# Optimization experiments

Hardware: AMD Instinct MI355X
Metric: run time of the kernel (lower is better)

Reference implementation:

```python
import jax, jax.numpy as jnp
import numpy as np

EMB = 1024
HEADS = 16
HEAD_DIM = EMB // HEADS
B, T = 2, 2048
LN_EPS = 1e-5  # torch nn.LayerNorm default


def _layernorm(x, g, b):
    # LayerNorm over last dim (head_dim), elementwise affine
    mu = jnp.mean(x, axis=-1, keepdims=True)
    var = jnp.mean(jnp.square(x - mu), axis=-1, keepdims=True)
    return (x - mu) * jax.lax.rsqrt(var + LN_EPS) * g + b


def setup_inputs() -> dict:
    key = jax.random.key(0)
    ks = jax.random.split(key, 6)
    sc = 1.0 / np.sqrt(EMB)  # keep linear outputs O(1)
    return {
        "x": jax.random.normal(ks[0], (B, T, EMB), dtype=jnp.float32),
        "Wk": jax.random.normal(ks[1], (EMB, EMB), dtype=jnp.float32) * sc,
        "Wq": jax.random.normal(ks[2], (EMB, EMB), dtype=jnp.float32) * sc,
        "Wv": jax.random.normal(ks[3], (EMB, EMB), dtype=jnp.float32) * sc,
        "Wu": jax.random.normal(ks[4], (EMB, EMB), dtype=jnp.float32) * sc,
        "bu": jnp.zeros((EMB,), dtype=jnp.float32),
        "kln_g": jnp.ones((HEAD_DIM,), dtype=jnp.float32),
        "kln_b": jnp.zeros((HEAD_DIM,), dtype=jnp.float32),
        "qln_g": jnp.ones((HEAD_DIM,), dtype=jnp.float32),
        "qln_b": jnp.zeros((HEAD_DIM,), dtype=jnp.float32),
    }


def reference(x, Wk, Wq, Wv, Wu, bu, kln_g, kln_b, qln_g, qln_b):
    b, t, e = x.shape
    h, s = HEADS, HEAD_DIM
    # torch Linear (no bias): y = x @ W.T
    keys = (x @ Wk.T).reshape(b, t, h, s)
    queries = (x @ Wq.T).reshape(b, t, h, s)
    values = (x @ Wv.T).reshape(b, t, h, s)
    # per-head LayerNorm (kqnorm=True)
    keys = _layernorm(keys, kln_g, kln_b)
    queries = _layernorm(queries, qln_g, qln_b)
    # NOTE: module scales by emb**(-1/4) on each side (net 1/sqrt(emb), not head dim)
    inv4 = e ** (-0.25)
    queries = queries * inv4
    keys = keys * inv4
    # scores: [b, h, t, t]
    dot = jnp.einsum('bqhs,bkhs->bhqk', queries, keys)
    # causal mask: positions k > q set to -inf (mask_diagonal=False -> diag kept)
    causal = jnp.tril(jnp.ones((t, t), dtype=bool))
    dot = jnp.where(causal, dot, -jnp.inf)
    attn = jax.nn.softmax(dot, axis=-1)
    out = jnp.einsum('bhqk,bkhs->bqhs', attn, values).reshape(b, t, h * s)
    return out @ Wu.T + bu
```

## Files before the change

### kernel.cpp

```cpp
#include <hip/hip_runtime.h>
#include <math.h>

#define EMB 1024
#define NHEADS 16
#define HDIM 64
#define BATCH 2
#define SEQ 2048
#define MROWS (BATCH*SEQ)
#define LN_EPS 1e-5f
#define GK 1024
#define GN 1024

typedef __attribute__((ext_vector_type(8))) short bf16x8;
typedef __attribute__((ext_vector_type(4))) short s16x4;
typedef __attribute__((ext_vector_type(4))) float f32x4;
typedef __attribute__((ext_vector_type(16))) float f32x16;
typedef __attribute__((ext_vector_type(4))) int int4v;

__device__ __forceinline__ short f2bf(float f) {
    union { float f; unsigned u; } v; v.f = f;
    unsigned r = v.u + 0x7FFFu + ((v.u >> 16) & 1u);
    return (short)(r >> 16);
}
__device__ __forceinline__ float bf2f(short s) {
    union { unsigned u; float f; } v; v.u = ((unsigned)(unsigned short)s) << 16;
    return v.f;
}
__device__ __forceinline__ void fsplit(float f, short& hi, short& lo) {
    const unsigned u = __float_as_uint(f);
    hi = (short)(u >> 16);
    const float r = f - __uint_as_float(u & 0xFFFF0000u);
    lo = (short)(__float_as_uint(r) >> 16);
}
__device__ __forceinline__ unsigned pk2(short a, short b) {
    return (unsigned)(unsigned short)a | ((unsigned)(unsigned short)b << 16);
}
__device__ __forceinline__ float fexp2(float x) {
    return __builtin_amdgcn_exp2f(x);
}

__device__ __forceinline__ void gload16(const short* g, short* l) {
    __builtin_amdgcn_global_load_lds(
        (const __attribute__((address_space(1))) unsigned*)g,
        (__attribute__((address_space(3))) unsigned*)l, 16, 0, 0);
}

#define MFMA32(a, b, c) __builtin_amdgcn_mfma_f32_32x32x16_bf16(a, b, c, 0, 0, 0)

#define SRC_G(r, c)  ((((c) - ((r) >> 1)) & 3) * 8)
#define RD_G(r, l4)  ((((l4) + ((r) >> 1)) & 3) * 8)

__global__ __launch_bounds__(256)
void cvt_all(const float* __restrict__ X, short* __restrict__ XH,
             const float* __restrict__ W0, const float* __restrict__ W1,
             const float* __restrict__ W2, const float* __restrict__ W3,
             short* __restrict__ WH)
{
    const int zy = blockIdx.y;
    if (zy == 0) {
        const size_t i = (size_t)blockIdx.x * 1024 + threadIdx.x * 4;
        const float4 v = *(const float4*)&X[i];
        s16x4 h;
        h[0] = f2bf(v.x); h[1] = f2bf(v.y);
        h[2] = f2bf(v.z); h[3] = f2bf(v.w);
        *(s16x4*)&XH[i] = h;
    } else {
        const int z = zy - 1;
        if (blockIdx.x >= 1024) return;
        const float* W = (z == 0) ? W0 : (z == 1) ? W1 : (z == 2) ? W2 : W3;
        const size_t i = (size_t)blockIdx.x * 1024 + threadIdx.x * 4;
        const float4 v = *(const float4*)&W[i];
        s16x4 h;
        h[0] = f2bf(v.x); h[1] = f2bf(v.y);
        h[2] = f2bf(v.z); h[3] = f2bf(v.w);
        *(s16x4*)&WH[((size_t)z << 20) + i] = h;
    }
}

__global__ __launch_bounds__(256, 3)
void gemm_kqv(const short* __restrict__ Xh, const short* __restrict__ W4h,
              const float* __restrict__ kg, const float* __restrict__ kb,
              const float* __restrict__ qg, const float* __restrict__ qb,
              float scaleK, float scaleQ,
              short* __restrict__ KhP,
              short* __restrict__ QhP, short* __restrict__ QlP,
              short* __restrict__ VTh)
{
    __shared__ short AhS[2][128][32], BhS[2][128][32];

    const int t   = threadIdx.x;
    const int ln  = t & 63, wv = t >> 6;
    const int l15 = ln & 15, l4 = ln >> 4;
    const int m0  = blockIdx.y * 128;
    const int n0  = blockIdx.x * 128;
    const int z   = blockIdx.z;
    const int wr  = (wv >> 1) * 64, wc = (wv & 1) * 64;

    const short* Bh = W4h + ((size_t)z << 20);

    const short* gplane = (wv < 2) ? Xh : Bh;
    const int    grow0  = (wv < 2) ? m0 : n0;
    short* lbase = (wv < 2) ? &AhS[0][0][0] : &BhS[0][0][0];
    const int s0 = (wv & 1) ? 4 : 0;

    f32x4 acc[4][4];
    #pragma unroll
    for (int i = 0; i < 4; ++i)
        #pragma unroll
        for (int j = 0; j < 4; ++j) acc[i][j] = (f32x4){0.f, 0.f, 0.f, 0.f};

    #pragma unroll
    for (int s = 0; s < 4; ++s) {
        const int chunk = (s0 + s) * 64 + ln;
        const int r = chunk >> 2, c = chunk & 3;
        gload16(gplane + (size_t)(grow0 + r) * GK + SRC_G(r, c),
                lbase + (s0 + s) * 512);
    }
    __syncthreads();

    int cur = 0;
    for (int k0 = 0; k0 < GK; k0 += 32) {
        if (k0 + 32 < GK) {
            short* lp = lbase + (cur ^ 1) * 4096;
            #pragma unroll
            for (int s = 0; s < 4; ++s) {
                const int chunk = (s0 + s) * 64 + ln;
                const int r = chunk >> 2, c = chunk & 3;
                gload16(gplane + (size_t)(grow0 + r) * GK + k0 + 32 + SRC_G(r, c),
                        lp + (s0 + s) * 512);
            }
        }

        bf16x8 ah[4], bh[4];
        #pragma unroll
        for (int f = 0; f < 4; ++f) {
            const int ra = wr + f * 16 + l15;
            const int rb = wc + f * 16 + l15;
            ah[f] = *(const bf16x8*)&AhS[cur][ra][RD_G(ra, l4)];
            bh[f] = *(const bf16x8*)&BhS[cur][rb][RD_G(rb, l4)];
        }
        #pragma unroll
        for (int i = 0; i < 4; ++i)
            #pragma unroll
            for (int j = 0; j < 4; ++j)
                acc[i][j] = __builtin_amdgcn_mfma_f32_16x16x32_bf16(ah[i], bh[j], acc[i][j], 0, 0, 0);

        __syncthreads();
        cur ^= 1;
    }

    if (z < 2) {
        const float* gamma = (z == 0) ? kg : qg;
        const float* beta  = (z == 0) ? kb : qb;
        short* OutH = (z == 0) ? KhP : QhP;
        const float scl = (z == 0) ? scaleK : scaleQ;
        const int n_head = (n0 + wc) >> 6;
        float g4[4], b4[4];
        #pragma unroll
        for (int f = 0; f < 4; ++f) {
            g4[f] = gamma[f * 16 + l15];
            b4[f] = beta [f * 16 + l15];
        }
        #pragma unroll
        for (int i = 0; i < 4; ++i)
            #pragma unroll
            for (int j = 0; j < 4; ++j) {
                const float v0 = acc[i][0][j], v1 = acc[i][1][j];
                const float v2 = acc[i][2][j], v3 = acc[i][3][j];
                float s1 = v0 + v1 + v2 + v3;
                float s2 = v0*v0 + v1*v1 + v2*v2 + v3*v3;
                s1 += __shfl_xor(s1, 1); s2 += __shfl_xor(s2, 1);
                s1 += __shfl_xor(s1, 2); s2 += __shfl_xor(s2, 2);
                s1 += __shfl_xor(s1, 4); s2 += __shfl_xor(s2, 4);
                s1 += __shfl_xor(s1, 8); s2 += __shfl_xor(s2, 8);
                const float mu  = s1 * (1.f / 64.f);
                const float var = s2 * (1.f / 64.f) - mu * mu;
                const float rs  = rsqrtf(var + LN_EPS);
                const int m = m0 + wr + i * 16 + l4 * 4 + j;
                const size_t orow =
                    ((size_t)((m >> 11) * NHEADS + n_head) * SEQ + (m & (SEQ - 1))) * HDIM;
                #pragma unroll
                for (int f = 0; f < 4; ++f) {
                    const float y = ((acc[i][f][j] - mu) * rs * g4[f] + b4[f]) * scl;
                    if (z == 0) {
                        OutH[orow + f * 16 + l15] = f2bf(y);
                    } else {
                        short hi, lo; fsplit(y, hi, lo);
                        OutH[orow + f * 16 + l15] = hi;
                        QlP [orow + f * 16 + l15] = lo;
                    }
                }
            }
    } else {
        #pragma unroll
        for (int i = 0; i < 4; ++i)
            #pragma unroll
            for (int f = 0; f < 4; ++f) {
                s16x4 h4;
                #pragma unroll
                for (int j = 0; j < 4; ++j) h4[j] = f2bf(acc[i][f][j]);
                const int n  = n0 + wc + f * 16 + l15;
                const int hh = n >> 6, dd = n & 63;
                const int mb = m0 + wr + i * 16 + l4 * 4;
                const size_t oa =
                    (((size_t)((mb >> 11) * NHEADS + hh)) * HDIM + dd) * SEQ + (mb & (SEQ - 1));
                *(s16x4*)&VTh[oa] = h4;
            }
    }
}

__global__ __launch_bounds__(256, 2)
void gemm_out(const short* __restrict__ Ah, const short* __restrict__ Bh,
              const float* __restrict__ bias, float* __restrict__ OutF)
{
    __shared__ short AhS[2][64][32], BhS[2][128][32];

    const int t   = threadIdx.x;
    const int ln  = t & 63, wv = t >> 6;
    const int l15 = ln & 15, l4 = ln >> 4;
    const int m0  = blockIdx.y * 64;
    const int n0  = blockIdx.x * 128;
    const int wr  = (wv >> 1) * 32, wc = (wv & 1) * 64;

    const short* gplane = (wv == 0) ? Ah : Bh;
    const int    grow0  = (wv == 0) ? m0 : n0;
    const int    s0     = (wv == 2) ? 4 : 0;
    const int    nseg   = (wv < 3) ? 4 : 0;
    const int    bstep  = (wv == 0) ? 2048 : 4096;
    short* lbase = (wv == 0) ? &AhS[0][0][0] : &BhS[0][0][0];

    f32x4 acc[2][4];
    #pragma unroll
    for (int i = 0; i < 2; ++i)
        #pragma unroll
        for (int j = 0; j < 4; ++j) acc[i][j] = (f32x4){0.f, 0.f, 0.f, 0.f};

    for (int s = 0; s < nseg; ++s) {
        const int chunk = (s0 + s) * 64 + ln;
        const int r = chunk >> 2, c = chunk & 3;
        gload16(gplane + (size_t)(grow0 + r) * GK + SRC_G(r, c),
                lbase + (s0 + s) * 512);
    }
    __syncthreads();

    int cur = 0;
    for (int k0 = 0; k0 < GK; k0 += 32) {
        if (k0 + 32 < GK) {
            short* lp = lbase + (cur ^ 1) * bstep;
            for (int s = 0; s < nseg; ++s) {
                const int chunk = (s0 + s) * 64 + ln;
                const int r = chunk >> 2, c = chunk & 3;
                gload16(gplane + (size_t)(grow0 + r) * GK + k0 + 32 + SRC_G(r, c),
                        lp + (s0 + s) * 512);
            }
        }

        bf16x8 ah[2], bh[4];
        #pragma unroll
        for (int f = 0; f < 2; ++f) {
            const int ra = wr + f * 16 + l15;
            ah[f] = *(const bf16x8*)&AhS[cur][ra][RD_G(ra, l4)];
        }
        #pragma unroll
        for (int f = 0; f < 4; ++f) {
            const int rb = wc + f * 16 + l15;
            bh[f] = *(const bf16x8*)&BhS[cur][rb][RD_G(rb, l4)];
        }
        #pragma unroll
        for (int i = 0; i < 2; ++i)
            #pragma unroll
            for (int j = 0; j < 4; ++j)
                acc[i][j] = __builtin_amdgcn_mfma_f32_16x16x32_bf16(ah[i], bh[j], acc[i][j], 0, 0, 0);

        __syncthreads();
        cur ^= 1;
    }

    float b4[4];
    #pragma unroll
    for (int f = 0; f < 4; ++f) b4[f] = bias[n0 + wc + f * 16 + l15];
    #pragma unroll
    for (int i = 0; i < 2; ++i)
        #pragma unroll
        for (int j = 0; j < 4; ++j) {
            const int m = m0 + wr + i * 16 + l4 * 4 + j;
            const size_t row = (size_t)m * GN + n0 + wc;
            #pragma unroll
            for (int f = 0; f < 4; ++f)
                OutF[row + f * 16 + l15] = acc[i][f][j] + b4[f];
        }
}

__global__ __launch_bounds__(256, 2)
void attn_mfma(const short* __restrict__ Qh, const short* __restrict__ Ql,
               const short* __restrict__ Kh, const short* __restrict__ Vh,
               short* __restrict__ Oh)
{
    __shared__ short KhS[64][64];
    __shared__ short VhS[64][64];

    const int t    = threadIdx.x;
    const int lane = t & 63, wv = t >> 6;
    const int l31  = lane & 31, hb = lane >> 5;
    const int bh   = blockIdx.y;
    const int bb   = bh >> 4, hh = bh & 15;
    const int qt   = bb ? (int)blockIdx.x
                        : (int)gridDim.x - 1 - (int)blockIdx.x;
    const int q0   = qt * 128;
    const int wq0  = wv * 32;

    const size_t kpan = (size_t)bh * SEQ * HDIM;
    const size_t vpan = (size_t)bh * HDIM * SEQ;

    const int sr0  = t >> 3, sr1 = 32 + (t >> 3);
    const int scg  = t & 7;
    const int soff = scg * 8;
    const int lc0  = (scg ^ (sr0 & 7)) * 8;
    const int lc1  = (scg ^ (sr1 & 7)) * 8;

    bf16x8 qfh[4], qfl[4];
    {
        const size_t qrow = kpan + (size_t)(q0 + wq0 + l31) * HDIM;
        #pragma unroll
        for (int ds = 0; ds < 4; ++ds) {
            qfh[ds] = *(const bf16x8*)&Qh[qrow + ds * 16 + hb * 8];
            qfl[ds] = *(const bf16x8*)&Ql[qrow + ds * 16 + hb * 8];
        }
    }

    f32x16 oacc0 = (f32x16)(0.0f), oacc1 = (f32x16)(0.0f);
    float m_run = -1e30f, l_run = 0.f;

    const int NT = 2 * qt + 2;

    int4v pKh0, pKh1, pVh0, pVh1;
    {
        pKh0 = *(const int4v*)&Kh[kpan + (size_t)sr0 * HDIM + soff];
        pKh1 = *(const int4v*)&Kh[kpan + (size_t)sr1 * HDIM + soff];
        pVh0 = *(const int4v*)&Vh[vpan + (size_t)sr0 * SEQ + soff];
        pVh1 = *(const int4v*)&Vh[vpan + (size_t)sr1 * SEQ + soff];
    }

    for (int kt = 0; kt < NT; ++kt) {
        const int k0 = kt * 64;

        __syncthreads();

        *(int4v*)&KhS[sr0][lc0] = pKh0;  *(int4v*)&KhS[sr1][lc1] = pKh1;
        *(int4v*)&VhS[sr0][lc0] = pVh0;  *(int4v*)&VhS[sr1][lc1] = pVh1;

        if (kt + 1 < NT) {
            const int kn = k0 + 64;
            pKh0 = *(const int4v*)&Kh[kpan + (size_t)(kn + sr0) * HDIM + soff];
            pKh1 = *(const int4v*)&Kh[kpan + (size_t)(kn + sr1) * HDIM + soff];
            pVh0 = *(const int4v*)&Vh[vpan + (size_t)sr0 * SEQ + kn + soff];
            pVh1 = *(const int4v*)&Vh[vpan + (size_t)sr1 * SEQ + kn + soff];
        }
        __syncthreads();

        if (k0 > q0 + wq0 + 31) continue;

        f32x16 s0 = (f32x16)(0.0f), s1 = (f32x16)(0.0f);
        #pragma unroll
        for (int ds = 0; ds < 4; ++ds) {
            const int g = ((ds * 2 + hb) ^ (l31 & 7)) * 8;
            const bf16x8 kh0 = *(const bf16x8*)&KhS[l31][g];
            const bf16x8 kh1 = *(const bf16x8*)&KhS[32 + l31][g];
            s0 = MFMA32(kh0, qfh[ds], s0);
            s0 = MFMA32(kh0, qfl[ds], s0);
            s1 = MFMA32(kh1, qfh[ds], s1);
            s1 = MFMA32(kh1, qfl[ds], s1);
        }

        if (k0 + 63 > q0 + wq0) {
            const int qg = q0 + wq0 + l31;
            #pragma unroll
            for (int reg = 0; reg < 16; ++reg) {
                const int kk = k0 + (reg & 3) + 8 * (reg >> 2) + 4 * hb;
                if (kk > qg)      s0[reg] = -1e30f;
                if (kk + 32 > qg) s1[reg] = -1e30f;
            }
        }

        {
            float mx = -1e30f;
            #pragma unroll
            for (int reg = 0; reg < 16; ++reg)
                mx = fmaxf(mx, fmaxf(s0[reg], s1[reg]));
            mx = fmaxf(mx, __shfl_xor(mx, 32));
            const float mnew = fmaxf(m_run, mx);
            const float scf  = fexp2(m_run - mnew);
            m_run = mnew;
            float ls = 0.f;
            #pragma unroll
            for (int reg = 0; reg < 16; ++reg) {
                const float p0 = fexp2(s0[reg] - mnew);
                const float p1 = fexp2(s1[reg] - mnew);
                s0[reg] = p0; s1[reg] = p1;
                ls += p0 + p1;
            }
            ls += __shfl_xor(ls, 32);
            l_run = l_run * scf + ls;
            #pragma unroll
            for (int reg = 0; reg < 16; ++reg) {
                oacc0[reg] *= scf;
                oacc1[reg] *= scf;
            }
        }

        #pragma unroll
        for (int ks = 0; ks < 4; ++ks) {
            short h8[8];
            #pragma unroll
            for (int a = 0; a < 8; ++a) {
                const float p = (ks >= 2) ? s1[(ks & 1) * 8 + a]
                                          : s0[(ks & 1) * 8 + a];
                h8[a] = f2bf(p);
            }
            const unsigned hA0 = pk2(h8[0], h8[1]), hA1 = pk2(h8[2], h8[3]);
            const unsigned hB0 = pk2(h8[4], h8[5]), hB1 = pk2(h8[6], h8[7]);
            const unsigned hr0 = (unsigned)__shfl_xor((int)(hb ? hA0 : hB0), 32);
            const unsigned hr1 = (unsigned)__shfl_xor((int)(hb ? hA1 : hB1), 32);
            const int4v wih = (int4v){(int)(hb ? hr0 : hA0), (int)(hb ? hr1 : hA1),
                                      (int)(hb ? hB0 : hr0), (int)(hb ? hB1 : hr1)};
            const bf16x8 pfh = __builtin_bit_cast(bf16x8, wih);

            const int gv = ((ks * 2 + hb) ^ (l31 & 7)) * 8;
            const bf16x8 vh0 = *(const bf16x8*)&VhS[l31][gv];
            const bf16x8 vh1 = *(const bf16x8*)&VhS[32 + l31][gv];
            oacc0 = MFMA32(vh0, pfh, oacc0);
            oacc1 = MFMA32(vh1, pfh, oacc1);
        }
    }

    const float inv = 1.f / l_run;
    const int q = q0 + wq0 + l31;
    const size_t row = ((size_t)(bb * SEQ + q)) * EMB + hh * HDIM;
    #pragma unroll
    for (int db = 0; db < 2; ++db)
        #pragma unroll
        for (int b = 0; b < 4; ++b) {
            s16x4 h4;
            #pragma unroll
            for (int a = 0; a < 4; ++a)
                h4[a] = f2bf((db ? oacc1[4 * b + a] : oacc0[4 * b + a]) * inv);
            const int d0 = db * 32 + 8 * b + 4 * hb;
            *(s16x4*)&Oh[row + d0] = h4;
        }
}

extern "C" void kernel_launch(void* const* d_in, const int* in_sizes, int n_in,
                              void* d_out, int out_size, void* d_ws, size_t ws_size,
                              hipStream_t stream)
{
    const float* x  = (const float*)d_in[0];
    const float* Wk = (const float*)d_in[1];
    const float* Wq = (const float*)d_in[2];
    const float* Wv = (const float*)d_in[3];
    const float* Wu = (const float*)d_in[4];
    const float* bu = (const float*)d_in[5];
    const float* kg = (const float*)d_in[6];
    const float* kb = (const float*)d_in[7];
    const float* qg = (const float*)d_in[8];
    const float* qb = (const float*)d_in[9];
    float* out = (float*)d_out;

    char* w = (char*)d_ws;
    short* XhP = (short*)(w);
    short* KhP = (short*)(w + (8u  << 20));
    short* QhP = (short*)(w + (16u << 20));
    short* QlP = (short*)(w + (24u << 20));
    short* W4h = (short*)(w + (32u << 20));
    short* VTh = (short*)d_out;

    const float inv4 = 0.17677669529663687f;
    const float l2e  = 1.4426950408889634f;

    cvt_all<<<dim3(4096, 5), 256, 0, stream>>>(x, XhP, Wk, Wq, Wv, Wu, W4h);

    gemm_kqv<<<dim3(GN / 128, MROWS / 128, 3), 256, 0, stream>>>(
        XhP, W4h, kg, kb, qg, qb, inv4, inv4 * l2e,
        KhP, QhP, QlP, VTh);

    attn_mfma<<<dim3(SEQ / 128, BATCH * NHEADS), 256, 0, stream>>>(
        QhP, QlP, KhP, VTh, XhP);

    gemm_out<<<dim3(GN / 128, MROWS / 64), 256, 0, stream>>>(
        XhP, W4h + (3u << 20), bu, out);
}
```

Before: 124.2 us.

## Triple-buffer LDS in QKV GEMM with partial vmcnt waits

Switches the fused QKV projection GEMM from double to triple buffering of the A/B shared-memory tiles, prefetching two k-steps ahead. Full __syncthreads is replaced by s_waitcnt vmcnt(4) plus a raw barrier, so one batch of global-to-LDS loads stays in flight while the next tile is computed. This aims to hide global load latency, at the cost of 50% more LDS per block, which may reduce occupancy under the 3-blocks launch bound.

New measurement: 125.6 us. About the same (+1.1%).

```diff
diff --git a/kernel.cpp b/kernel.cpp
--- a/kernel.cpp
+++ b/kernel.cpp
@@ -86,7 +86,7 @@
               short* __restrict__ QhP, short* __restrict__ QlP,
               short* __restrict__ VTh)
 {
-    __shared__ short AhS[2][128][32], BhS[2][128][32];
+    __shared__ short AhS[3][128][32], BhS[3][128][32];
 
     const int t   = threadIdx.x;
     const int ln  = t & 63, wv = t >> 6;
@@ -116,17 +116,27 @@
         gload16(gplane + (size_t)(grow0 + r) * GK + SRC_G(r, c),
                 lbase + (s0 + s) * 512);
     }
-    __syncthreads();
+    #pragma unroll
+    for (int s = 0; s < 4; ++s) {
+        const int chunk = (s0 + s) * 64 + ln;
+        const int r = chunk >> 2, c = chunk & 3;
+        gload16(gplane + (size_t)(grow0 + r) * GK + 32 + SRC_G(r, c),
+                lbase + 4096 + (s0 + s) * 512);
+    }
+    asm volatile("s_waitcnt vmcnt(4)" ::: "memory");
+    __builtin_amdgcn_s_barrier();
 
     int cur = 0;
-    for (int k0 = 0; k0 < GK; k0 += 32) {
-        if (k0 + 32 < GK) {
-            short* lp = lbase + (cur ^ 1) * 4096;
+    for (int i = 0; i < 32; ++i) {
+        const int cur2 = (cur == 0) ? 2 : cur - 1;
+        if (i + 2 < 32) {
+            short* lp = lbase + cur2 * 4096;
+            const int kof = (i + 2) * 32;
             #pragma unroll
             for (int s = 0; s < 4; ++s) {
                 const int chunk = (s0 + s) * 64 + ln;
                 const int r = chunk >> 2, c = chunk & 3;
-                gload16(gplane + (size_t)(grow0 + r) * GK + k0 + 32 + SRC_G(r, c),
+                gload16(gplane + (size_t)(grow0 + r) * GK + kof + SRC_G(r, c),
                         lp + (s0 + s) * 512);
             }
         }
@@ -140,13 +150,18 @@
             bh[f] = *(const bf16x8*)&BhS[cur][rb][RD_G(rb, l4)];
         }
         #pragma unroll
-        for (int i = 0; i < 4; ++i)
+        for (int i2 = 0; i2 < 4; ++i2)
             #pragma unroll
             for (int j = 0; j < 4; ++j)
-                acc[i][j] = __builtin_amdgcn_mfma_f32_16x16x32_bf16(ah[i], bh[j], acc[i][j], 0, 0, 0);
-
-        __syncthreads();
-        cur ^= 1;
+                acc[i2][j] = __builtin_amdgcn_mfma_f32_16x16x32_bf16(ah[i2], bh[j], acc[i2][j], 0, 0, 0);
+
+        if (i + 2 < 32) {
+            asm volatile("s_waitcnt vmcnt(4)" ::: "memory");
+        } else if (i + 1 < 32) {
+            asm volatile("s_waitcnt vmcnt(0)" ::: "memory");
+        }
+        __builtin_amdgcn_s_barrier();
+        cur = (cur == 2) ? 0 : cur + 1;
     }
 
     if (z < 2) {
```
